# Kernel optimization log

Hardware: AMD Instinct MI355X
Metric: run time of the kernel (lower is better)

Reference implementation:

```python
import jax, jax.numpy as jnp
import numpy as np


def _ln(x, g, b, eps=1e-5):
    m = x.mean(-1, keepdims=True)
    v = x.var(-1, keepdims=True)
    return (x - m) / jnp.sqrt(v + eps) * g + b


def setup_inputs() -> dict:
    key = jax.random.key(0)
    ks = jax.random.split(key, 10)
    N, H, E, OUT, L = 4096, 256, 131072, 64, 6
    s = 1.0 / np.sqrt(H)
    return {
        "x": jax.random.normal(ks[0], (N, H), jnp.float32),
        "edge_index": jax.random.randint(ks[1], (2, E), 0, N, jnp.int32),
        "sage_wl": jax.random.normal(ks[2], (L, H, H), jnp.float32) * s,   # lin_l (neighbors, has bias)
        "sage_wr": jax.random.normal(ks[3], (L, H, H), jnp.float32) * s,   # lin_r (root, no bias)
        "sage_bl": jnp.zeros((L, H), jnp.float32),
        "ln_g": jnp.ones((L - 1, H), jnp.float32),
        "ln_b": jnp.zeros((L - 1, H), jnp.float32),
        "conv_w": jax.random.normal(ks[4], (3, H, H, 3), jnp.float32) * (1.0 / np.sqrt(3 * H)),  # [layer,O,I,K]
        "conv_b": jnp.zeros((3, H), jnp.float32),
        "cnorm_g": jnp.ones((3, H), jnp.float32),
        "cnorm_b": jnp.zeros((3, H), jnp.float32),
        "in_proj_w": jax.random.normal(ks[5], (6 * H, 2 * H), jnp.float32) * (1.0 / np.sqrt(2 * H)),
        "in_proj_b": jnp.zeros((6 * H,), jnp.float32),
        "out_proj_w": jax.random.normal(ks[6], (2 * H, 2 * H), jnp.float32) * (1.0 / np.sqrt(2 * H)),
        "out_proj_b": jnp.zeros((2 * H,), jnp.float32),
        "anorm_g": jnp.ones((2 * H,), jnp.float32),
        "anorm_b": jnp.zeros((2 * H,), jnp.float32),
        "fuse_w": jax.random.normal(ks[7], (OUT, 2 * H), jnp.float32) * (1.0 / np.sqrt(2 * H)),
        "fuse_b": jnp.zeros((OUT,), jnp.float32),
    }


def reference(x, edge_index, sage_wl, sage_wr, sage_bl, ln_g, ln_b,
              conv_w, conv_b, cnorm_g, cnorm_b,
              in_proj_w, in_proj_b, out_proj_w, out_proj_b,
              anorm_g, anorm_b, fuse_w, fuse_b):
    # Dropout layers act as identity (eval mode).
    N, H = x.shape
    L = sage_wl.shape[0]
    src, dst = edge_index[0], edge_index[1]
    deg = jax.ops.segment_sum(jnp.ones(src.shape[0], x.dtype), dst, num_segments=N)
    deg = jnp.maximum(deg, 1.0)[:, None]
    h = x
    for i in range(L):
        res = h
        # SAGEConv: mean-aggregate neighbor features (gather/scatter), then two linears
        agg = jax.ops.segment_sum(h[src], dst, num_segments=N) / deg
        h = agg @ sage_wl[i].T + sage_bl[i] + h @ sage_wr[i].T
        if i < L - 1:
            h = _ln(h, ln_g[i], ln_b[i])
        h = jax.nn.relu(h) + res  # residual (shapes always match: in==hidden)
    gnn_out = h                                   # [N, H]

    # CNN branch over the node axis: [1, H, N]
    c = gnn_out.T[None]
    for j in range(3):
        c = jax.lax.conv_general_dilated(c, conv_w[j], (1,), ((1, 1),),
                                         dimension_numbers=("NCH", "OIH", "NCH"))
        c = jax.nn.relu(c + conv_b[j][None, :, None])
        c = _ln(c.transpose(0, 2, 1), cnorm_g[j], cnorm_b[j]).transpose(0, 2, 1)
    cnn_out = c[0].T                              # [N, H]

    fused = jnp.concatenate([gnn_out, cnn_out], axis=1)  # [N, 2H]
    E2 = fused.shape[1]
    heads = 4
    hd = E2 // heads
    qkv = fused @ in_proj_w.T + in_proj_b
    q, k, v = jnp.split(qkv, 3, axis=1)
    split_heads = lambda t: t.reshape(N, heads, hd).transpose(1, 0, 2)  # [h, N, hd]
    q, k, v = split_heads(q), split_heads(k), split_heads(v)
    scores = jnp.einsum("hnd,hmd->hnm", q, k) / np.sqrt(hd).astype(np.float32)
    a = jax.nn.softmax(scores, axis=-1)
    o = jnp.einsum("hnm,hmd->hnd", a, v).transpose(1, 0, 2).reshape(N, E2)
    o = o @ out_proj_w.T + out_proj_b
    o = _ln(o, anorm_g, anorm_b)
    return o @ fuse_w.T + fuse_b                  # [N, out_channels]
```

## Files before the change

kernel.cpp:

```cpp
#include <hip/hip_runtime.h>

#define NN 4096
#define HH 256
#define EE 131072

__device__ __constant__ float LN_EPS = 1e-5f;
#define ATT_SCALE 0.08838834764831845f
#define ATT_SHIFT 30.0f

typedef __attribute__((ext_vector_type(8))) short bf16x8_t;
typedef __attribute__((ext_vector_type(4))) float f32x4_t;

__device__ inline ushort f2b(float f) {
  uint u = __float_as_uint(f);
  uint r = (u + 0x7FFF + ((u >> 16) & 1)) >> 16;
  return (ushort)r;
}

__global__ void hist_kernel(const int* __restrict__ ei, int* __restrict__ cnt) {
  int e = blockIdx.x * blockDim.x + threadIdx.x;
  if (e < EE) atomicAdd(&cnt[ei[EE + e]], 1);
}

__global__ __launch_bounds__(1024) void scan_kernel(int* __restrict__ cnt_cursor,
                                                    int* __restrict__ rowptr,
                                                    float* __restrict__ invdeg) {
  __shared__ int part[1024];
  int t = threadIdx.x;
  int base = t * 4;
  int cs[4];
  int s = 0;
  for (int u = 0; u < 4; ++u) { cs[u] = cnt_cursor[base + u]; s += cs[u]; }
  part[t] = s;
  __syncthreads();
  for (int off = 1; off < 1024; off <<= 1) {
    int add = (t >= off) ? part[t - off] : 0;
    int v = part[t];
    __syncthreads();
    part[t] = v + add;
    __syncthreads();
  }
  int excl = (t > 0) ? part[t - 1] : 0;
  for (int u = 0; u < 4; ++u) {
    rowptr[base + u] = excl;
    cnt_cursor[base + u] = excl;
    invdeg[base + u] = 1.0f / (float)max(cs[u], 1);
    excl += cs[u];
  }
  if (t == 1023) rowptr[NN] = excl;
}

__global__ void fill_kernel(const int* __restrict__ ei, int* __restrict__ cursor,
                            int* __restrict__ col) {
  int e = blockIdx.x * blockDim.x + threadIdx.x;
  if (e < EE) {
    int d = ei[EE + e];
    int p = atomicAdd(&cursor[d], 1);
    col[p] = ei[e];
  }
}

__global__ __launch_bounds__(256) void castw(const float* __restrict__ in,
                                             ushort* __restrict__ out) {
  int i4 = (blockIdx.x * 256 + threadIdx.x) * 4;
  float4 v = *(const float4*)(in + i4);
  ushort4 w;
  w.x = f2b(v.x); w.y = f2b(v.y); w.z = f2b(v.z); w.w = f2b(v.w);
  *(ushort4*)(out + i4) = w;
}

__global__ __launch_bounds__(256) void castconv(const float* __restrict__ w,
                                                ushort* __restrict__ o) {
  int idx = blockIdx.x * 256 + threadIdx.x;
  int j = idx / 196608;
  int rem = idx - j * 196608;
  int oc = rem / 768;
  int kk = rem - oc * 768;
  int ks = kk >> 8, ii = kk & 255;
  o[idx] = f2b(w[j * 196608 + oc * 768 + ii * 3 + ks]);
}

__global__ __launch_bounds__(64) void agg_kernel(const float* __restrict__ h,
                                                 const int* __restrict__ rowptr,
                                                 const int* __restrict__ col,
                                                 const float* __restrict__ invdeg,
                                                 ushort* __restrict__ aggb) {
  int n = blockIdx.x;
  int t = threadIdx.x;
  int s = rowptr[n], e = rowptr[n + 1];
  float4 acc = make_float4(0.f, 0.f, 0.f, 0.f);
  for (int j = s; j < e; ++j) {
    int c = col[j];
    const float4 v = *(const float4*)(h + (size_t)c * HH + t * 4);
    acc.x += v.x; acc.y += v.y; acc.z += v.z; acc.w += v.w;
  }
  float id = invdeg[n];
  ushort4 w;
  w.x = f2b(acc.x * id); w.y = f2b(acc.y * id);
  w.z = f2b(acc.z * id); w.w = f2b(acc.w * id);
  *(ushort4*)(aggb + (size_t)n * HH + t * 4) = w;
}

__global__ __launch_bounds__(256) void gemm_mfma(
    const ushort* __restrict__ A0, const ushort* __restrict__ A1,
    const ushort* __restrict__ B0, const ushort* __restrict__ B1,
    const float* __restrict__ bias, float* __restrict__ Cf, ushort* __restrict__ Cb,
    int M, int Nn, int K, int KHA, int KHB, int relu) {
  __shared__ ushort Alds[64][40];
  __shared__ ushort Blds[128][40];
  int t = threadIdx.x;
  int w = t >> 6, l = t & 63, quad = l >> 4, lr = l & 15;
  int wm = w & 1, wn = w >> 1;
  int m0 = blockIdx.x * 64, n0 = blockIdx.y * 128;
  int sr = t >> 2, sc8 = (t & 3) * 8;
  f32x4_t acc[2][4];
#pragma unroll
  for (int s = 0; s < 2; ++s)
#pragma unroll
    for (int q = 0; q < 4; ++q) acc[s][q] = (f32x4_t){0.f, 0.f, 0.f, 0.f};

  for (int k0 = 0; k0 < K; k0 += 32) {
    int kk = k0 + sc8;
    const ushort* ap = (kk < KHA) ? (A0 + (size_t)(m0 + sr) * KHA + kk)
                                  : (A1 + (size_t)(m0 + sr) * (K - KHA) + (kk - KHA));
    uint4 av = *(const uint4*)ap;
    const ushort* bp0 = (kk < KHB) ? (B0 + (size_t)(n0 + sr) * KHB + kk)
                                   : (B1 + (size_t)(n0 + sr) * (K - KHB) + (kk - KHB));
    uint4 bv0 = *(const uint4*)bp0;
    const ushort* bp1 = (kk < KHB) ? (B0 + (size_t)(n0 + 64 + sr) * KHB + kk)
                                   : (B1 + (size_t)(n0 + 64 + sr) * (K - KHB) + (kk - KHB));
    uint4 bv1 = *(const uint4*)bp1;
    __syncthreads();
    *(uint4*)&Alds[sr][sc8] = av;
    *(uint4*)&Blds[sr][sc8] = bv0;
    *(uint4*)&Blds[64 + sr][sc8] = bv1;
    __syncthreads();
    bf16x8_t af[2], bf[4];
#pragma unroll
    for (int s = 0; s < 2; ++s)
      af[s] = *(const bf16x8_t*)&Alds[wm * 32 + s * 16 + lr][quad * 8];
#pragma unroll
    for (int q = 0; q < 4; ++q)
      bf[q] = *(const bf16x8_t*)&Blds[wn * 64 + q * 16 + lr][quad * 8];
#pragma unroll
    for (int s = 0; s < 2; ++s)
#pragma unroll
      for (int q = 0; q < 4; ++q)
        acc[s][q] = __builtin_amdgcn_mfma_f32_16x16x32_bf16(af[s], bf[q], acc[s][q], 0, 0, 0);
  }
#pragma unroll
  for (int s = 0; s < 2; ++s) {
#pragma unroll
    for (int q = 0; q < 4; ++q) {
      int n = n0 + wn * 64 + q * 16 + lr;
      float bb = bias[n];
#pragma unroll
      for (int r = 0; r < 4; ++r) {
        int m = m0 + wm * 32 + s * 16 + quad * 4 + r;
        float v = acc[s][q][r] + bb;
        if (relu) v = fmaxf(v, 0.f);
        if (Cf) Cf[(size_t)m * Nn + n] = v;
        if (Cb) Cb[(size_t)m * Nn + n] = f2b(v);
      }
    }
  }
}

__global__ __launch_bounds__(256) void gemm_conv_mfma(
    const ushort* __restrict__ Ab, const ushort* __restrict__ B,
    const float* __restrict__ bias, float* __restrict__ Cf) {
  __shared__ ushort Alds[64][40];
  __shared__ ushort Blds[128][40];
  int t = threadIdx.x;
  int w = t >> 6, l = t & 63, quad = l >> 4, lr = l & 15;
  int wm = w & 1, wn = w >> 1;
  int m0 = blockIdx.x * 64, n0 = blockIdx.y * 128;
  int sr = t >> 2, sc8 = (t & 3) * 8;
  f32x4_t acc[2][4];
#pragma unroll
  for (int s = 0; s < 2; ++s)
#pragma unroll
    for (int q = 0; q < 4; ++q) acc[s][q] = (f32x4_t){0.f, 0.f, 0.f, 0.f};

  for (int k0 = 0; k0 < 768; k0 += 32) {
    int kk = k0 + sc8;
    int ks = kk >> 8, ii = kk & 255;
    int nr = m0 + sr + ks - 1;
    uint4 av = make_uint4(0u, 0u, 0u, 0u);
    if (nr >= 0 && nr < NN) av = *(const uint4*)(Ab + (size_t)nr * HH + ii);
    uint4 bv0 = *(const uint4*)(B + (size_t)(n0 + sr) * 768 + kk);
    uint4 bv1 = *(const uint4*)(B + (size_t)(n0 + 64 + sr) * 768 + kk);
    __syncthreads();
    *(uint4*)&Alds[sr][sc8] = av;
    *(uint4*)&Blds[sr][sc8] = bv0;
    *(uint4*)&Blds[64 + sr][sc8] = bv1;
    __syncthreads();
    bf16x8_t af[2], bf[4];
#pragma unroll
    for (int s = 0; s < 2; ++s)
      af[s] = *(const bf16x8_t*)&Alds[wm * 32 + s * 16 + lr][quad * 8];
#pragma unroll
    for (int q = 0; q < 4; ++q)
      bf[q] = *(const bf16x8_t*)&Blds[wn * 64 + q * 16 + lr][quad * 8];
#pragma unroll
    for (int s = 0; s < 2; ++s)
#pragma unroll
      for (int q = 0; q < 4; ++q)
        acc[s][q] = __builtin_amdgcn_mfma_f32_16x16x32_bf16(af[s], bf[q], acc[s][q], 0, 0, 0);
  }
#pragma unroll
  for (int s = 0; s < 2; ++s) {
#pragma unroll
    for (int q = 0; q < 4; ++q) {
      int n = n0 + wn * 64 + q * 16 + lr;
      float bb = bias[n];
#pragma unroll
      for (int r = 0; r < 4; ++r) {
        int m = m0 + wm * 32 + s * 16 + quad * 4 + r;
        Cf[(size_t)m * HH + n] = fmaxf(acc[s][q][r] + bb, 0.f);
      }
    }
  }
}

__global__ __launch_bounds__(256) void gemm_std(
    const float* __restrict__ A0, const float* __restrict__ B0,
    const float* __restrict__ bias, float* __restrict__ C,
    int M, int Nn, int K) {
  __shared__ float As[16][68];
  __shared__ float Bs[16][68];
  int t = threadIdx.x;
  int m0 = blockIdx.x * 64, n0 = blockIdx.y * 64;
  int ty = t >> 4, tx = t & 15;
  int lr = t >> 2, lc4 = (t & 3) * 4;
  float acc[4][4] = {};
  for (int k0 = 0; k0 < K; k0 += 16) {
    int kk = k0 + lc4;
    float4 va = *(const float4*)(A0 + (size_t)(m0 + lr) * K + kk);
    As[lc4 + 0][lr] = va.x; As[lc4 + 1][lr] = va.y;
    As[lc4 + 2][lr] = va.z; As[lc4 + 3][lr] = va.w;
    float4 vb = *(const float4*)(B0 + (size_t)(n0 + lr) * K + kk);
    Bs[lc4 + 0][lr] = vb.x; Bs[lc4 + 1][lr] = vb.y;
    Bs[lc4 + 2][lr] = vb.z; Bs[lc4 + 3][lr] = vb.w;
    __syncthreads();
#pragma unroll
    for (int k = 0; k < 16; ++k) {
      float4 a4 = *(const float4*)&As[k][4 * ty];
      float4 b4 = *(const float4*)&Bs[k][4 * tx];
      float av[4] = {a4.x, a4.y, a4.z, a4.w};
      float bv[4] = {b4.x, b4.y, b4.z, b4.w};
#pragma unroll
      for (int i = 0; i < 4; ++i)
#pragma unroll
        for (int j = 0; j < 4; ++j) acc[i][j] += av[i] * bv[j];
    }
    __syncthreads();
  }
#pragma unroll
  for (int i = 0; i < 4; ++i) {
    int m = m0 + 4 * ty + i;
    float o[4];
#pragma unroll
    for (int j = 0; j < 4; ++j) o[j] = acc[i][j] + bias[n0 + 4 * tx + j];
    float4 o4 = make_float4(o[0], o[1], o[2], o[3]);
    *(float4*)(C + (size_t)m * Nn + n0 + 4 * tx) = o4;
  }
}

__global__ __launch_bounds__(256) void ln_fuse(
    const float* __restrict__ x, const float* __restrict__ g, const float* __restrict__ b,
    const float* __restrict__ res, float* __restrict__ outf, ushort* __restrict__ outb,
    int D, int do_ln, int relu_res) {
  int row = blockIdx.x, t = threadIdx.x;
  int nv = D >> 8;
  float vals[2];
  float s = 0.f, sq = 0.f;
  for (int u = 0; u < nv; ++u) {
    float v = x[(size_t)row * D + t + (u << 8)];
    vals[u] = v; s += v; sq += v * v;
  }
  __shared__ float red[8];
  float m = 0.f, inv = 1.f;
  if (do_ln) {
    for (int off = 32; off >= 1; off >>= 1) {
      s += __shfl_xor(s, off);
      sq += __shfl_xor(sq, off);
    }
    int wid = t >> 6;
    if ((t & 63) == 0) { red[wid] = s; red[4 + wid] = sq; }
    __syncthreads();
    if (t == 0) {
      float S = red[0] + red[1] + red[2] + red[3];
      float Q = red[4] + red[5] + red[6] + red[7];
      float mm = S / D;
      float vv = Q / D - mm * mm;
      red[0] = mm;
      red[1] = rsqrtf(vv + LN_EPS);
    }
    __syncthreads();
    m = red[0]; inv = red[1];
  }
  for (int u = 0; u < nv; ++u) {
    int c = t + (u << 8);
    float y = vals[u];
    if (do_ln) y = (y - m) * inv * g[c] + b[c];
    if (relu_res) y = fmaxf(y, 0.f) + res[(size_t)row * D + c];
    if (outf) outf[(size_t)row * D + c] = y;
    if (outb) outb[(size_t)row * D + c] = f2b(y);
  }
}

__global__ __launch_bounds__(256) void vtrans(const ushort* __restrict__ qkvb,
                                              ushort* __restrict__ Vt) {
  __shared__ ushort tile[32][34];
  int t = threadIdx.x;
  int n0 = blockIdx.x * 32, d0 = blockIdx.y * 32;
  int tx = t & 31, ty = t >> 5;
#pragma unroll
  for (int u = 0; u < 4; ++u) {
    int r = ty + 8 * u;
    tile[r][tx] = qkvb[(size_t)(n0 + r) * 1536 + 1024 + d0 + tx];
  }
  __syncthreads();
#pragma unroll
  for (int u = 0; u < 4; ++u) {
    int dy = ty + 8 * u;
    Vt[(size_t)(d0 + dy) * NN + n0 + tx] = tile[tx][dy];
  }
}

__global__ __launch_bounds__(128) void attn_mfma(const ushort* __restrict__ qkvb,
                                                 const ushort* __restrict__ Vt,
                                                 ushort* __restrict__ Ob) {
  __shared__ ushort Klds[64][136];
  __shared__ ushort Vlds[128][72];
  __shared__ ushort Plds[2][16][72];

  int t = threadIdx.x;
  int w = t >> 6, l = t & 63;
  int quad = l >> 4, lr = l & 15;
  int head = blockIdx.y;
  int q0 = blockIdx.x * 32;

  bf16x8_t qf[4];
#pragma unroll
  for (int ks = 0; ks < 4; ++ks)
    qf[ks] = *(const bf16x8_t*)(qkvb + (size_t)(q0 + w * 16 + lr) * 1536 + head * 128 +
                                ks * 32 + quad * 8);

  f32x4_t of[8];
#pragma unroll
  for (int dt = 0; dt < 8; ++dt) of[dt] = (f32x4_t){0.f, 0.f, 0.f, 0.f};
  float den[4] = {0.f, 0.f, 0.f, 0.f};

  for (int kt = 0; kt < NN / 64; ++kt) {
    int k0 = kt * 64;
    __syncthreads();
#pragma unroll
    for (int p = 0; p < 8; ++p) {
      int c0 = t + p * 128;
      int row = c0 >> 4, c8 = (c0 & 15) * 8;
      *(uint4*)&Klds[row][c8] =
          *(const uint4*)(qkvb + (size_t)(k0 + row) * 1536 + 512 + head * 128 + c8);
    }
#pragma unroll
    for (int p = 0; p < 8; ++p) {
      int c0 = t + p * 128;
      int row = c0 >> 3, kv8 = (c0 & 7) * 8;
      *(uint4*)&Vlds[row][kv8] =
          *(const uint4*)(Vt + (size_t)(head * 128 + row) * NN + k0 + kv8);
    }
    __syncthreads();

    f32x4_t sf[4];
#pragma unroll
    for (int ct = 0; ct < 4; ++ct) sf[ct] = (f32x4_t){0.f, 0.f, 0.f, 0.f};
#pragma unroll
    for (int ks = 0; ks < 4; ++ks) {
#pragma unroll
      for (int ct = 0; ct < 4; ++ct) {
        bf16x8_t kf = *(const bf16x8_t*)&Klds[ct * 16 + lr][ks * 32 + quad * 8];
        sf[ct] = __builtin_amdgcn_mfma_f32_16x16x32_bf16(qf[ks], kf, sf[ct], 0, 0, 0);
      }
    }

    float rs[4] = {0.f, 0.f, 0.f, 0.f};
#pragma unroll
    for (int ct = 0; ct < 4; ++ct) {
#pragma unroll
      for (int r = 0; r < 4; ++r) {
        float e = __expf(sf[ct][r] * ATT_SCALE - ATT_SHIFT);
        Plds[w][quad * 4 + r][ct * 16 + lr] = f2b(e);
        rs[r] += e;
      }
    }
#pragma unroll
    for (int mask = 1; mask < 16; mask <<= 1) {
#pragma unroll
      for (int r = 0; r < 4; ++r) rs[r] += __shfl_xor(rs[r], mask);
    }
#pragma unroll
    for (int r = 0; r < 4; ++r) den[r] += rs[r];

#pragma unroll
    for (int ks2 = 0; ks2 < 2; ++ks2) {
      bf16x8_t pf = *(const bf16x8_t*)&Plds[w][lr][ks2 * 32 + quad * 8];
#pragma unroll
      for (int dt = 0; dt < 8; ++dt) {
        bf16x8_t vf = *(const bf16x8_t*)&Vlds[dt * 16 + lr][ks2 * 32 + quad * 8];
        of[dt] = __builtin_amdgcn_mfma_f32_16x16x32_bf16(pf, vf, of[dt], 0, 0, 0);
      }
    }
  }

  float inv[4];
#pragma unroll
  for (int r = 0; r < 4; ++r) inv[r] = 1.0f / den[r];
#pragma unroll
  for (int dt = 0; dt < 8; ++dt) {
#pragma unroll
    for (int r = 0; r < 4; ++r) {
      int row = q0 + w * 16 + quad * 4 + r;
      Ob[(size_t)row * 512 + head * 128 + dt * 16 + lr] = f2b(of[dt][r] * inv[r]);
    }
  }
}

extern "C" void kernel_launch(void* const* d_in, const int* in_sizes, int n_in,
                              void* d_out, int out_size, void* d_ws, size_t ws_size,
                              hipStream_t stream) {
  const float* x          = (const float*)d_in[0];
  const int*   ei         = (const int*)d_in[1];
  const float* sage_wl    = (const float*)d_in[2];
  const float* sage_wr    = (const float*)d_in[3];
  const float* sage_bl    = (const float*)d_in[4];
  const float* ln_g       = (const float*)d_in[5];
  const float* ln_b       = (const float*)d_in[6];
  const float* conv_w     = (const float*)d_in[7];
  const float* conv_b     = (const float*)d_in[8];
  const float* cnorm_g    = (const float*)d_in[9];
  const float* cnorm_b    = (const float*)d_in[10];
  const float* in_proj_w  = (const float*)d_in[11];
  const float* in_proj_b  = (const float*)d_in[12];
  const float* out_proj_w = (const float*)d_in[13];
  const float* out_proj_b = (const float*)d_in[14];
  const float* anorm_g    = (const float*)d_in[15];
  const float* anorm_b    = (const float*)d_in[16];
  const float* fuse_w     = (const float*)d_in[17];
  const float* fuse_b     = (const float*)d_in[18];
  float* out = (float*)d_out;

  char* ws = (char*)d_ws;
  const size_t MB = 1 << 20;
  int*    rowptr = (int*)(ws + 0);
  int*    cnt    = (int*)(ws + 65536);
  int*    col    = (int*)(ws + 131072);
  float*  invdeg = (float*)(ws + 786432);
  float*  h    = (float*)(ws + 1 * MB);
  ushort* hb   = (ushort*)(ws + 5 * MB);
  ushort* aggb = (ushort*)(ws + 7 * MB);
  float*  tmp  = (float*)(ws + 9 * MB);
  ushort* c0b  = (ushort*)(ws + 13 * MB);
  ushort* c1b  = (ushort*)(ws + 15 * MB);
  ushort* qkvb = (ushort*)(ws + 17 * MB);
  float*  op   = (float*)(ws + 17 * MB);
  ushort* Vt   = (ushort*)(ws + 29 * MB);
  ushort* aob  = (ushort*)(ws + 33 * MB);
  ushort* wlb  = (ushort*)(ws + 37 * MB);
  ushort* wrb  = (ushort*)(ws + 37 * MB + 786432);
  ushort* cvb  = (ushort*)(ws + 37 * MB + 1572864);
  ushort* ipb  = (ushort*)(ws + 37 * MB + 2752512);
  ushort* opb  = (ushort*)(ws + 37 * MB + 4325376);

  castw<<<(6 * 256 * 256) / 1024, 256, 0, stream>>>(sage_wl, wlb);
  castw<<<(6 * 256 * 256) / 1024, 256, 0, stream>>>(sage_wr, wrb);
  castconv<<<(3 * 256 * 768) / 256, 256, 0, stream>>>(conv_w, cvb);
  castw<<<(1536 * 512) / 1024, 256, 0, stream>>>(in_proj_w, ipb);
  castw<<<(512 * 512) / 1024, 256, 0, stream>>>(out_proj_w, opb);

  hipMemsetAsync(cnt, 0, NN * sizeof(int), stream);
  hist_kernel<<<EE / 256, 256, 0, stream>>>(ei, cnt);
  scan_kernel<<<1, 1024, 0, stream>>>(cnt, rowptr, invdeg);
  fill_kernel<<<EE / 256, 256, 0, stream>>>(ei, cnt, col);
  hipMemcpyAsync(h, x, (size_t)NN * HH * sizeof(float), hipMemcpyDeviceToDevice, stream);
  castw<<<(NN * HH) / 1024, 256, 0, stream>>>(x, hb);

  for (int i = 0; i < 6; ++i) {
    agg_kernel<<<NN, 64, 0, stream>>>(h, rowptr, col, invdeg, aggb);
    gemm_mfma<<<dim3(64, 2), 256, 0, stream>>>(
        aggb, hb, wlb + (size_t)i * HH * HH, wrb + (size_t)i * HH * HH,
        sage_bl + i * HH, tmp, nullptr, NN, HH, 512, 256, 256, 0);
    int do_ln = (i < 5) ? 1 : 0;
    const float* gp = do_ln ? (ln_g + i * HH) : ln_g;
    const float* bp = do_ln ? (ln_b + i * HH) : ln_b;
    ln_fuse<<<NN, 256, 0, stream>>>(tmp, gp, bp, h, h, hb, HH, do_ln, 1);
  }

  const ushort* cin = hb;
  ushort* couts[3] = {c0b, c1b, c0b};
  for (int j = 0; j < 3; ++j) {
    gemm_conv_mfma<<<dim3(64, 2), 256, 0, stream>>>(
        cin, cvb + (size_t)j * HH * 768, conv_b + j * HH, tmp);
    ln_fuse<<<NN, 256, 0, stream>>>(tmp, cnorm_g + j * HH, cnorm_b + j * HH,
                                    nullptr, nullptr, couts[j], HH, 1, 0);
    cin = couts[j];
  }

  gemm_mfma<<<dim3(64, 12), 256, 0, stream>>>(
      hb, c0b, ipb, nullptr, in_proj_b, nullptr, qkvb, NN, 1536, 512, 256, 1536 * 0 + 512, 0);
  vtrans<<<dim3(NN / 32, 512 / 32), 256, 0, stream>>>(qkvb, Vt);
  attn_mfma<<<dim3(NN / 32, 4), 128, 0, stream>>>(qkvb, Vt, aob);

  gemm_mfma<<<dim3(64, 4), 256, 0, stream>>>(
      aob, nullptr, opb, nullptr, out_proj_b, op, nullptr, NN, 512, 512, 512, 512, 0);
  ln_fuse<<<NN, 256, 0, stream>>>(op, anorm_g, anorm_b, nullptr, op, nullptr, 512, 1, 0);
  gemm_std<<<dim3(64, 1), 256, 0, stream>>>(op, fuse_w, fuse_b, out, NN, 64, 512);
}
```

Baseline: 606.7 us.

## Restructure attention: direct global K/V fragments, 32 rows per wave, MFMA row-sum

The attention kernel now has each wave compute two 16-row query tiles. It loads K and V MFMA fragments directly from global memory instead of staging them through shared memory with block barriers. The softmax denominator is accumulated by an extra MFMA against a ones fragment, replacing the shuffle-based row reductions. This removes LDS staging and synchronisation and reuses each K/V fragment twice, but it halves the grid and relies on cache for the uncoalesced fragment loads.

```diff
diff --git a/kernel.cpp b/kernel.cpp
--- a/kernel.cpp
+++ b/kernel.cpp
@@ -329,101 +329,104 @@
   }
 }
 
-__global__ __launch_bounds__(128) void attn_mfma(const ushort* __restrict__ qkvb,
-                                                 const ushort* __restrict__ Vt,
-                                                 ushort* __restrict__ Ob) {
-  __shared__ ushort Klds[64][136];
-  __shared__ ushort Vlds[128][72];
-  __shared__ ushort Plds[2][16][72];
+__global__ __launch_bounds__(128, 1) void attn_mfma(const ushort* __restrict__ qkvb,
+                                                    const ushort* __restrict__ Vt,
+                                                    ushort* __restrict__ Ob) {
+  __shared__ ushort Plds[2][32][72];
 
   int t = threadIdx.x;
   int w = t >> 6, l = t & 63;
   int quad = l >> 4, lr = l & 15;
   int head = blockIdx.y;
-  int q0 = blockIdx.x * 32;
-
-  bf16x8_t qf[4];
-#pragma unroll
-  for (int ks = 0; ks < 4; ++ks)
-    qf[ks] = *(const bf16x8_t*)(qkvb + (size_t)(q0 + w * 16 + lr) * 1536 + head * 128 +
-                                ks * 32 + quad * 8);
-
-  f32x4_t of[8];
-#pragma unroll
-  for (int dt = 0; dt < 8; ++dt) of[dt] = (f32x4_t){0.f, 0.f, 0.f, 0.f};
-  float den[4] = {0.f, 0.f, 0.f, 0.f};
+  int q0 = blockIdx.x * 64 + w * 32;
+
+  bf16x8_t qf[2][4];
+#pragma unroll
+  for (int s = 0; s < 2; ++s)
+#pragma unroll
+    for (int ks = 0; ks < 4; ++ks)
+      qf[s][ks] = *(const bf16x8_t*)(qkvb + (size_t)(q0 + s * 16 + lr) * 1536 + head * 128 +
+                                     ks * 32 + quad * 8);
+
+  bf16x8_t onesf;
+  {
+    short ov = (lr == 0) ? (short)0x3F80 : (short)0;
+#pragma unroll
+    for (int j = 0; j < 8; ++j) onesf[j] = ov;
+  }
+
+  f32x4_t of[2][8];
+  f32x4_t oden[2];
+#pragma unroll
+  for (int s = 0; s < 2; ++s) {
+    oden[s] = (f32x4_t){0.f, 0.f, 0.f, 0.f};
+#pragma unroll
+    for (int dt = 0; dt < 8; ++dt) of[s][dt] = (f32x4_t){0.f, 0.f, 0.f, 0.f};
+  }
+
+  const ushort* kbase = qkvb + 512 + head * 128 + quad * 8;
+  const ushort* vbase = Vt + (size_t)head * 128 * NN + quad * 8;
 
   for (int kt = 0; kt < NN / 64; ++kt) {
     int k0 = kt * 64;
-    __syncthreads();
-#pragma unroll
-    for (int p = 0; p < 8; ++p) {
-      int c0 = t + p * 128;
-      int row = c0 >> 4, c8 = (c0 & 15) * 8;
-      *(uint4*)&Klds[row][c8] =
-          *(const uint4*)(qkvb + (size_t)(k0 + row) * 1536 + 512 + head * 128 + c8);
-    }
-#pragma unroll
-    for (int p = 0; p < 8; ++p) {
-      int c0 = t + p * 128;
-      int row = c0 >> 3, kv8 = (c0 & 7) * 8;
-      *(uint4*)&Vlds[row][kv8] =
-          *(const uint4*)(Vt + (size_t)(head * 128 + row) * NN + k0 + kv8);
-    }
-    __syncthreads();
-
-    f32x4_t sf[4];
-#pragma unroll
-    for (int ct = 0; ct < 4; ++ct) sf[ct] = (f32x4_t){0.f, 0.f, 0.f, 0.f};
+
+    f32x4_t sf[2][4];
+#pragma unroll
+    for (int s = 0; s < 2; ++s)
+#pragma unroll
+      for (int ct = 0; ct < 4; ++ct) sf[s][ct] = (f32x4_t){0.f, 0.f, 0.f, 0.f};
 #pragma unroll
     for (int ks = 0; ks < 4; ++ks) {
 #pragma unroll
       for (int ct = 0; ct < 4; ++ct) {
-        bf16x8_t kf = *(const bf16x8_t*)&Klds[ct * 16 + lr][ks * 32 + quad * 8];
-        sf[ct] = __builtin_amdgcn_mfma_f32_16x16x32_bf16(qf[ks], kf, sf[ct], 0, 0, 0);
+        bf16x8_t kf = *(const bf16x8_t*)(kbase + (size_t)(k0 + ct * 16 + lr) * 1536 + ks * 32);
+        sf[0][ct] = __builtin_amdgcn_mfma_f32_16x16x32_bf16(qf[0][ks], kf, sf[0][ct], 0, 0, 0);
+        sf[1][ct] = __builtin_amdgcn_mfma_f32_16x16x32_bf16(qf[1][ks], kf, sf[1][ct], 0, 0, 0);
       }
     }
 
-    float rs[4] = {0.f, 0.f, 0.f, 0.f};
-#pragma unroll
-    for (int ct = 0; ct < 4; ++ct) {
+#pragma unroll
+    for (int s = 0; s < 2; ++s)
+#pragma unroll
+      for (int ct = 0; ct < 4; ++ct)
+#pragma unroll
+        for (int r = 0; r < 4; ++r) {
+          float e = __expf(sf[s][ct][r] * ATT_SCALE - ATT_SHIFT);
+          Plds[w][s * 16 + quad * 4 + r][ct * 16 + lr] = f2b(e);
+        }
+
+#pragma unroll
+    for (int ks2 = 0; ks2 < 2; ++ks2) {
+      bf16x8_t pf0 = *(const bf16x8_t*)&Plds[w][lr][ks2 * 32 + quad * 8];
+      bf16x8_t pf1 = *(const bf16x8_t*)&Plds[w][16 + lr][ks2 * 32 + quad * 8];
+      oden[0] = __builtin_amdgcn_mfma_f32_16x16x32_bf16(pf0, onesf, oden[0], 0, 0, 0);
+      oden[1] = __builtin_amdgcn_mfma_f32_16x16x32_bf16(pf1, onesf, oden[1], 0, 0, 0);
+#pragma unroll
+      for (int dt = 0; dt < 8; ++dt) {
+        bf16x8_t vf = *(const bf16x8_t*)(vbase + (size_t)(dt * 16 + lr) * NN + k0 + ks2 * 32);
+        of[0][dt] = __builtin_amdgcn_mfma_f32_16x16x32_bf16(pf0, vf, of[0][dt], 0, 0, 0);
+        of[1][dt] = __builtin_amdgcn_mfma_f32_16x16x32_bf16(pf1, vf, of[1][dt], 0, 0, 0);
+      }
+    }
+  }
+
+  float inv[2][4];
+#pragma unroll
+  for (int s = 0; s < 2; ++s)
+#pragma unroll
+    for (int r = 0; r < 4; ++r) {
+      float d = __shfl(oden[s][r], (l & 48));
+      inv[s][r] = 1.0f / d;
+    }
+#pragma unroll
+  for (int s = 0; s < 2; ++s)
+#pragma unroll
+    for (int dt = 0; dt < 8; ++dt)
 #pragma unroll
       for (int r = 0; r < 4; ++r) {
-        float e = __expf(sf[ct][r] * ATT_SCALE - ATT_SHIFT);
-        Plds[w][quad * 4 + r][ct * 16 + lr] = f2b(e);
-        rs[r] += e;
+        int row = q0 + s * 16 + quad * 4 + r;
+        Ob[(size_t)row * 512 + head * 128 + dt * 16 + lr] = f2b(of[s][dt][r] * inv[s][r]);
       }
-    }
-#pragma unroll
-    for (int mask = 1; mask < 16; mask <<= 1) {
-#pragma unroll
-      for (int r = 0; r < 4; ++r) rs[r] += __shfl_xor(rs[r], mask);
-    }
-#pragma unroll
-    for (int r = 0; r < 4; ++r) den[r] += rs[r];
-
-#pragma unroll
-    for (int ks2 = 0; ks2 < 2; ++ks2) {
-      bf16x8_t pf = *(const bf16x8_t*)&Plds[w][lr][ks2 * 32 + quad * 8];
-#pragma unroll
-      for (int dt = 0; dt < 8; ++dt) {
-        bf16x8_t vf = *(const bf16x8_t*)&Vlds[dt * 16 + lr][ks2 * 32 + quad * 8];
-        of[dt] = __builtin_amdgcn_mfma_f32_16x16x32_bf16(pf, vf, of[dt], 0, 0, 0);
-      }
-    }
-  }
-
-  float inv[4];
-#pragma unroll
-  for (int r = 0; r < 4; ++r) inv[r] = 1.0f / den[r];
-#pragma unroll
-  for (int dt = 0; dt < 8; ++dt) {
-#pragma unroll
-    for (int r = 0; r < 4; ++r) {
-      int row = q0 + w * 16 + quad * 4 + r;
-      Ob[(size_t)row * 512 + head * 128 + dt * 16 + lr] = f2b(of[dt][r] * inv[r]);
-    }
-  }
 }
 
 extern "C" void kernel_launch(void* const* d_in, const int* in_sizes, int n_in,
@@ -507,9 +510,9 @@
   }
 
   gemm_mfma<<<dim3(64, 12), 256, 0, stream>>>(
-      hb, c0b, ipb, nullptr, in_proj_b, nullptr, qkvb, NN, 1536, 512, 256, 1536 * 0 + 512, 0);
+      hb, c0b, ipb, nullptr, in_proj_b, nullptr, qkvb, NN, 1536, 512, 256, 512, 0);
   vtrans<<<dim3(NN / 32, 512 / 32), 256, 0, stream>>>(qkvb, Vt);
-  attn_mfma<<<dim3(NN / 32, 4), 128, 0, stream>>>(qkvb, Vt, aob);
+  attn_mfma<<<dim3(NN / 64, 4), 128, 0, stream>>>(qkvb, Vt, aob);
 
   gemm_mfma<<<dim3(64, 4), 256, 0, stream>>>(
       aob, nullptr, opb, nullptr, out_proj_b, op, nullptr, NN, 512, 512, 512, 512, 0);
```

Result: slower. 814.2 us (+34.2%).
